# Optimization experiments

Hardware: AMD Instinct MI355X
Metric: run time of the kernel (lower is better)

The kernel has to match this reference:

```python
import jax, jax.numpy as jnp
import numpy as np

D_NODE, D_EDGE, D_HEAD = 256, 128, 32
LN_EPS = 1e-5


def setup_inputs() -> dict:
    key = jax.random.key(0)
    ks = jax.random.split(key, 10)
    B, N = 1, 512
    s_node = 1.0 / np.sqrt(D_NODE)
    s_hh = 1.0 / np.sqrt(D_HEAD * D_HEAD)
    return {
        "node": jax.random.normal(ks[0], (B, N, D_NODE), dtype=jnp.float32),
        "edge": jax.random.normal(ks[1], (B, N, N, D_EDGE), dtype=jnp.float32),
        "ln_w": jnp.ones((D_NODE,), dtype=jnp.float32),
        "ln_b": jnp.zeros((D_NODE,), dtype=jnp.float32),
        "w_left": jax.random.normal(ks[2], (D_NODE, D_HEAD), dtype=jnp.float32) * s_node,
        "b_left": jax.random.normal(ks[3], (D_HEAD,), dtype=jnp.float32) * 0.02,
        "w_right": jax.random.normal(ks[4], (D_NODE, D_HEAD), dtype=jnp.float32) * s_node,
        "b_right": jax.random.normal(ks[5], (D_HEAD,), dtype=jnp.float32) * 0.02,
        "w_out": jax.random.normal(ks[6], (D_HEAD * D_HEAD, D_EDGE), dtype=jnp.float32) * s_hh,
        "b_out": jax.random.normal(ks[7], (D_EDGE,), dtype=jnp.float32) * 0.02,
    }


def reference(node, edge, ln_w, ln_b, w_left, b_left, w_right, b_right, w_out, b_out):
    # LayerNorm over d_node
    mu = jnp.mean(node, axis=-1, keepdims=True)
    var = jnp.mean(jnp.square(node - mu), axis=-1, keepdims=True)
    x = (node - mu) * jax.lax.rsqrt(var + LN_EPS) * ln_w + ln_b

    left = x @ w_left + b_left    # [B, N, d_head]
    right = x @ w_right + b_right  # [B, N, d_head]

    # Outer product flattened over (i,j) then projected to d_edge.
    # Fused: reshape w_out to [i, j, e] and contract directly, avoiding the
    # explicit [B, N, N, d_head*d_head] intermediate (same math as
    # einsum('bni,bmj->bnmij').flatten(-2) @ w_out).
    w3 = w_out.reshape(D_HEAD, D_HEAD, D_EDGE)
    out = jnp.einsum("bni,bmj,ije->bnme", left, right, w3) + b_out
    return out + edge
```

## Files before the change

kernel.cpp:

```cpp
#include <hip/hip_runtime.h>

#define D_NODE 256
#define D_EDGE 128
#define D_HEAD 32
#define NN 512

typedef float f4v __attribute__((ext_vector_type(4)));

__global__ __launch_bounds__(256) void ln_proj_kernel(
    const float* __restrict__ node, const float* __restrict__ ln_w,
    const float* __restrict__ ln_b, const float* __restrict__ w_left,
    const float* __restrict__ b_left, const float* __restrict__ w_right,
    const float* __restrict__ b_right, float* __restrict__ left,
    float* __restrict__ right) {
  __shared__ float xs[D_NODE];
  __shared__ float red[10];
  __shared__ float part[4][64];
  const int n = blockIdx.x;
  const int t = threadIdx.x;
  float v = node[n * D_NODE + t];
  float s = v, ss = v * v;
#pragma unroll
  for (int o = 32; o > 0; o >>= 1) {
    s += __shfl_down(s, o);
    ss += __shfl_down(ss, o);
  }
  if ((t & 63) == 0) {
    red[t >> 6] = s;
    red[4 + (t >> 6)] = ss;
  }
  __syncthreads();
  if (t == 0) {
    float S = red[0] + red[1] + red[2] + red[3];
    float SS = red[4] + red[5] + red[6] + red[7];
    float mu = S * (1.0f / D_NODE);
    float var = SS * (1.0f / D_NODE) - mu * mu;
    red[8] = mu;
    red[9] = rsqrtf(var + 1e-5f);
  }
  __syncthreads();
  const float mu = red[8], rs = red[9];
  xs[t] = (v - mu) * rs * ln_w[t] + ln_b[t];
  __syncthreads();
  {
    const int col = t & 63;
    const int q = t >> 6;
    const int c = col & 31;
    const float* w = (col < 32) ? w_left : w_right;
    float acc = 0.f;
    const int d0 = q * 64;
#pragma unroll 8
    for (int d = d0; d < d0 + 64; ++d) acc = fmaf(xs[d], w[d * D_HEAD + c], acc);
    part[q][col] = acc;
  }
  __syncthreads();
  if (t < 64) {
    const int c = t & 31;
    const bool isL = (t < 32);
    float acc = part[0][t] + part[1][t] + part[2][t] + part[3][t] +
                (isL ? b_left[c] : b_right[c]);
    (isL ? left : right)[n * D_HEAD + c] = acc;
  }
}

__global__ __launch_bounds__(256) void rw_kernel(
    const float* __restrict__ right, const float* __restrict__ w_out,
    float* __restrict__ tmp) {
  const int m0 = blockIdx.x * 4;
  const int i = blockIdx.y * 8 + (threadIdx.x >> 5);
  const int e4 = threadIdx.x & 31;
  const float4* wp = (const float4*)(w_out + i * D_HEAD * D_EDGE) + e4;
  const float* r = right + m0 * D_HEAD;
  float4 a0 = {0, 0, 0, 0}, a1 = {0, 0, 0, 0}, a2 = {0, 0, 0, 0},
         a3 = {0, 0, 0, 0};
#pragma unroll
  for (int j = 0; j < D_HEAD; ++j) {
    const float4 w4 = wp[j * (D_EDGE / 4)];
    const float r0 = r[j], r1 = r[32 + j], r2 = r[64 + j], r3 = r[96 + j];
    a0.x = fmaf(r0, w4.x, a0.x); a0.y = fmaf(r0, w4.y, a0.y);
    a0.z = fmaf(r0, w4.z, a0.z); a0.w = fmaf(r0, w4.w, a0.w);
    a1.x = fmaf(r1, w4.x, a1.x); a1.y = fmaf(r1, w4.y, a1.y);
    a1.z = fmaf(r1, w4.z, a1.z); a1.w = fmaf(r1, w4.w, a1.w);
    a2.x = fmaf(r2, w4.x, a2.x); a2.y = fmaf(r2, w4.y, a2.y);
    a2.z = fmaf(r2, w4.z, a2.z); a2.w = fmaf(r2, w4.w, a2.w);
    a3.x = fmaf(r3, w4.x, a3.x); a3.y = fmaf(r3, w4.y, a3.y);
    a3.z = fmaf(r3, w4.z, a3.z); a3.w = fmaf(r3, w4.w, a3.w);
  }
  ((float4*)(tmp + ((m0 + 0) * D_HEAD + i) * D_EDGE))[e4] = a0;
  ((float4*)(tmp + ((m0 + 1) * D_HEAD + i) * D_EDGE))[e4] = a1;
  ((float4*)(tmp + ((m0 + 2) * D_HEAD + i) * D_EDGE))[e4] = a2;
  ((float4*)(tmp + ((m0 + 3) * D_HEAD + i) * D_EDGE))[e4] = a3;
}

__global__ __launch_bounds__(256) void fuse_kernel(
    const float* __restrict__ left, const float* __restrict__ tmp,
    const float* __restrict__ b_out, const float* __restrict__ edge,
    float* __restrict__ out) {
  __shared__ float tl[2 * D_HEAD * D_EDGE];
  const int m0 = blockIdx.x * 2;
  const int t = threadIdx.x;
  {
    const float4* ts = (const float4*)(tmp + m0 * D_HEAD * D_EDGE);
    float4* td = (float4*)tl;
#pragma unroll
    for (int k = 0; k < 8; ++k) td[t + 256 * k] = ts[t + 256 * k];
  }
  const int lane = t & 63;
  const int wv = __builtin_amdgcn_readfirstlane(t >> 6);
  const int e4 = lane & 31;
  const int mh = lane >> 5;
  const int n0 = blockIdx.y * 128 + wv * 32;
  const float4 be = ((const float4*)b_out)[e4];
  const float* tb = tl + mh * (D_HEAD * D_EDGE) + e4 * 4;
  const float4* edge4 = (const float4*)edge;
  float4* out4 = (float4*)out;
  const int rowstr = NN * (D_EDGE / 4);
  const int base = (n0 * NN + m0) * (D_EDGE / 4) + lane;

  float4 eb[2][8];
#pragma unroll
  for (int r = 0; r < 8; ++r) eb[0][r] = edge4[base + r * rowstr];
  __syncthreads();

#pragma unroll
  for (int g = 0; g < 4; ++g) {
    const int cur = g & 1;
    const int gb = base + g * 8 * rowstr;
    if (g < 3) {
#pragma unroll
      for (int r = 0; r < 8; ++r)
        eb[cur ^ 1][r] = edge4[gb + (8 + r) * rowstr];
    }
    float4 acc[8];
#pragma unroll
    for (int r = 0; r < 8; ++r) acc[r] = be;
    const float* lp = left + (n0 + g * 8) * D_HEAD;
#pragma unroll 4
    for (int i = 0; i < D_HEAD; ++i) {
      const float4 tv = *(const float4*)(tb + i * D_EDGE);
#pragma unroll
      for (int r = 0; r < 8; ++r) {
        const float l = lp[r * D_HEAD + i];
        acc[r].x = fmaf(l, tv.x, acc[r].x);
        acc[r].y = fmaf(l, tv.y, acc[r].y);
        acc[r].z = fmaf(l, tv.z, acc[r].z);
        acc[r].w = fmaf(l, tv.w, acc[r].w);
      }
    }
#pragma unroll
    for (int r = 0; r < 8; ++r) {
      acc[r].x += eb[cur][r].x;
      acc[r].y += eb[cur][r].y;
      acc[r].z += eb[cur][r].z;
      acc[r].w += eb[cur][r].w;
      __builtin_nontemporal_store(*(const f4v*)&acc[r],
                                  (f4v*)(out4 + gb + r * rowstr));
    }
  }
}

extern "C" void kernel_launch(void* const* d_in, const int* in_sizes, int n_in,
                              void* d_out, int out_size, void* d_ws, size_t ws_size,
                              hipStream_t stream) {
  const float* node    = (const float*)d_in[0];
  const float* edge    = (const float*)d_in[1];
  const float* ln_w    = (const float*)d_in[2];
  const float* ln_b    = (const float*)d_in[3];
  const float* w_left  = (const float*)d_in[4];
  const float* b_left  = (const float*)d_in[5];
  const float* w_right = (const float*)d_in[6];
  const float* b_right = (const float*)d_in[7];
  const float* w_out   = (const float*)d_in[8];
  const float* b_out   = (const float*)d_in[9];
  float* out = (float*)d_out;

  float* left  = (float*)d_ws;
  float* right = left + NN * D_HEAD;
  float* tmp   = right + NN * D_HEAD;

  ln_proj_kernel<<<NN, 256, 0, stream>>>(node, ln_w, ln_b, w_left, b_left,
                                         w_right, b_right, left, right);
  rw_kernel<<<dim3(NN / 4, 4), 256, 0, stream>>>(right, w_out, tmp);
  fuse_kernel<<<dim3(NN / 2, 4), 256, 0, stream>>>(left, tmp, b_out, edge, out);
}
```

Measured before the change: 271.3 us.

## Split fuse kernel into smaller blocks with XCD-aware mapping, drop LDS staging

Launches the fuse kernel as a 1D grid of 4096 small blocks, each handling 8 rows per wave, instead of 1024 blocks with four software-pipelined row groups. Block IDs are remapped so that blocks sharing an m-pair land on the same XCD, which improves L2 reuse of the tmp slice. The tmp slice is now read straight from global/L2 rather than staged in shared memory. The edge prefetch double-buffering and the barrier are removed in favour of more concurrent blocks hiding latency. The cost is redundant tmp reads per block and no explicit overlap of loads with compute.

```diff
diff --git a/kernel.cpp b/kernel.cpp
--- a/kernel.cpp
+++ b/kernel.cpp
@@ -96,67 +96,52 @@
     const float* __restrict__ left, const float* __restrict__ tmp,
     const float* __restrict__ b_out, const float* __restrict__ edge,
     float* __restrict__ out) {
-  __shared__ float tl[2 * D_HEAD * D_EDGE];
-  const int m0 = blockIdx.x * 2;
+  const int bid = blockIdx.x;
+  const int xcd = bid & 7;
+  const int rr = bid >> 3;
+  const int p = (xcd << 5) | (rr & 31);
+  const int chunk = rr >> 5;
+  const int m0 = p * 2;
   const int t = threadIdx.x;
-  {
-    const float4* ts = (const float4*)(tmp + m0 * D_HEAD * D_EDGE);
-    float4* td = (float4*)tl;
-#pragma unroll
-    for (int k = 0; k < 8; ++k) td[t + 256 * k] = ts[t + 256 * k];
-  }
   const int lane = t & 63;
-  const int wv = __builtin_amdgcn_readfirstlane(t >> 6);
+  const int wv = t >> 6;
   const int e4 = lane & 31;
   const int mh = lane >> 5;
-  const int n0 = blockIdx.y * 128 + wv * 32;
+  const int n0 = chunk * 32 + wv * 8;
+
   const float4 be = ((const float4*)b_out)[e4];
-  const float* tb = tl + mh * (D_HEAD * D_EDGE) + e4 * 4;
+  const float4* tp = (const float4*)(tmp + (m0 + mh) * (D_HEAD * D_EDGE)) + e4;
   const float4* edge4 = (const float4*)edge;
   float4* out4 = (float4*)out;
   const int rowstr = NN * (D_EDGE / 4);
   const int base = (n0 * NN + m0) * (D_EDGE / 4) + lane;
 
-  float4 eb[2][8];
+  float4 acc[8];
 #pragma unroll
-  for (int r = 0; r < 8; ++r) eb[0][r] = edge4[base + r * rowstr];
-  __syncthreads();
-
+  for (int q = 0; q < 8; ++q) {
+    const float4 ev = edge4[base + q * rowstr];
+    acc[q].x = be.x + ev.x;
+    acc[q].y = be.y + ev.y;
+    acc[q].z = be.z + ev.z;
+    acc[q].w = be.w + ev.w;
+  }
+  const float* lp = left + n0 * D_HEAD;
+#pragma unroll 4
+  for (int i = 0; i < D_HEAD; ++i) {
+    const float4 tv = tp[i * (D_EDGE / 4)];
 #pragma unroll
-  for (int g = 0; g < 4; ++g) {
-    const int cur = g & 1;
-    const int gb = base + g * 8 * rowstr;
-    if (g < 3) {
-#pragma unroll
-      for (int r = 0; r < 8; ++r)
-        eb[cur ^ 1][r] = edge4[gb + (8 + r) * rowstr];
-    }
-    float4 acc[8];
-#pragma unroll
-    for (int r = 0; r < 8; ++r) acc[r] = be;
-    const float* lp = left + (n0 + g * 8) * D_HEAD;
-#pragma unroll 4
-    for (int i = 0; i < D_HEAD; ++i) {
-      const float4 tv = *(const float4*)(tb + i * D_EDGE);
-#pragma unroll
-      for (int r = 0; r < 8; ++r) {
-        const float l = lp[r * D_HEAD + i];
-        acc[r].x = fmaf(l, tv.x, acc[r].x);
-        acc[r].y = fmaf(l, tv.y, acc[r].y);
-        acc[r].z = fmaf(l, tv.z, acc[r].z);
-        acc[r].w = fmaf(l, tv.w, acc[r].w);
-      }
-    }
-#pragma unroll
-    for (int r = 0; r < 8; ++r) {
-      acc[r].x += eb[cur][r].x;
-      acc[r].y += eb[cur][r].y;
-      acc[r].z += eb[cur][r].z;
-      acc[r].w += eb[cur][r].w;
-      __builtin_nontemporal_store(*(const f4v*)&acc[r],
-                                  (f4v*)(out4 + gb + r * rowstr));
+    for (int q = 0; q < 8; ++q) {
+      const float l = lp[q * D_HEAD + i];
+      acc[q].x = fmaf(l, tv.x, acc[q].x);
+      acc[q].y = fmaf(l, tv.y, acc[q].y);
+      acc[q].z = fmaf(l, tv.z, acc[q].z);
+      acc[q].w = fmaf(l, tv.w, acc[q].w);
     }
   }
+#pragma unroll
+  for (int q = 0; q < 8; ++q)
+    __builtin_nontemporal_store(*(const f4v*)&acc[q],
+                                (f4v*)(out4 + base + q * rowstr));
 }
 
 extern "C" void kernel_launch(void* const* d_in, const int* in_sizes, int n_in,
@@ -181,5 +166,5 @@
   ln_proj_kernel<<<NN, 256, 0, stream>>>(node, ln_w, ln_b, w_left, b_left,
                                          w_right, b_right, left, right);
   rw_kernel<<<dim3(NN / 4, 4), 256, 0, stream>>>(right, w_out, tmp);
-  fuse_kernel<<<dim3(NN / 2, 4), 256, 0, stream>>>(left, tmp, b_out, edge, out);
+  fuse_kernel<<<dim3(NN * 8), 256, 0, stream>>>(left, tmp, b_out, edge, out);
 }
```

Result: slower. 287.5 us (+6.0%).
